# Optimization experiments

Hardware: AMD Instinct MI355X
Metric: run time of the kernel (lower is better)

Reference implementation:

```python
import jax, jax.numpy as jnp
import numpy as np

B, NTS, NOS_F, NTS_F, H, A, HIST = 8192, 64, 7, 6, 64, 9, 2


def _lstm(x, Wih, Whh, bih, bhh):
    # x: [B, T, in] -> all hidden states [B, T, H]; torch gate order (i, f, g, o)
    xg = jnp.einsum('bti,gi->btg', x, Wih) + bih + bhh  # precompute input projection
    Hh = Whh.shape[1]

    def step(carry, xt):
        h, c = carry
        gates = xt + h @ Whh.T
        i, f, g, o = jnp.split(gates, 4, axis=-1)
        c = jax.nn.sigmoid(f) * c + jax.nn.sigmoid(i) * jnp.tanh(g)
        h = jax.nn.sigmoid(o) * jnp.tanh(c)
        return (h, c), h

    z = jnp.zeros((x.shape[0], Hh), x.dtype)
    _, hs = jax.lax.scan(step, (z, z), jnp.swapaxes(xg, 0, 1))
    return jnp.swapaxes(hs, 0, 1)


def _inner(s, WOS, bOS, Wih, Whh, bih, bhh, WTS, bTS):
    # NaN-masked ragged TS sequences + dynamic last-valid-step gather
    b = s.shape[0]
    sOS = s[:, :NOS_F]
    sTS = s[:, NOS_F:].reshape(b, -1, NTS_F)
    nan = jnp.isnan(sTS)
    n = jnp.sum(~nan[:, :, 0], axis=1)          # valid TS count per row
    h_idx = jnp.maximum(n - 1, 0)
    sTS = jnp.where(nan, 0.0, sTS)
    xOS = jax.nn.relu(sOS @ WOS.T + bOS)
    hs = _lstm(sTS, Wih, Whh, bih, bhh)
    xTS = hs[jnp.arange(b), h_idx]              # hidden state at last valid step
    xTS = jax.nn.relu(xTS @ WTS.T + bTS)
    return jnp.concatenate([xOS, xTS], axis=1)  # [B, 128]


def setup_inputs() -> dict:
    key = jax.random.key(0)
    ks = iter(jax.random.split(key, 48))

    def nanify(x, k):  # NaN-pad beyond a random valid prefix length in [1, NTS]
        lens = jax.random.randint(k, x.shape[:-2], 1, NTS + 1)
        mask = jnp.arange(NTS) < lens[..., None]
        return jnp.where(mask[..., None], x, jnp.nan)

    sTS = nanify(jax.random.normal(next(ks), (B, NTS, NTS_F)), next(ks))
    s = jnp.concatenate([jax.random.normal(next(ks), (B, NOS_F)), sTS.reshape(B, -1)], axis=1)
    shTS = nanify(jax.random.normal(next(ks), (B, HIST, NTS, NTS_F)), next(ks))
    s_hist = jnp.concatenate([jax.random.normal(next(ks), (B, HIST, NOS_F)), shTS.reshape(B, HIST, -1)], axis=2)
    hist_len = jax.random.randint(next(ks), (B,), 0, HIST + 1)
    a_hist = jnp.zeros((B, HIST, 1), jnp.float32)

    p = lambda *shape: jax.random.normal(next(ks), shape, jnp.float32) * 0.1
    inp = dict(s=s, s_hist=s_hist, a_hist=a_hist, hist_len=hist_len)
    for t in (0, 1, 2):
        inp[f'WOS{t}'] = p(H, NOS_F); inp[f'bOS{t}'] = p(H)
        inp[f'Wih{t}'] = p(4 * H, NTS_F); inp[f'Whh{t}'] = p(4 * H, H)
        inp[f'bih{t}'] = p(4 * H); inp[f'bhh{t}'] = p(4 * H)
        inp[f'WTS{t}'] = p(H, H); inp[f'bTS{t}'] = p(H)
    inp['Wiho'] = p(4 * H, 2 * H); inp['Whho'] = p(4 * H, H)
    inp['biho'] = p(4 * H); inp['bhho'] = p(4 * H)
    inp['W1'] = p(H, H); inp['b1'] = p(H)
    inp['W2'] = p(A, H); inp['b2'] = p(A)
    return inp


def reference(s, s_hist, a_hist, hist_len,
              WOS0, bOS0, Wih0, Whh0, bih0, bhh0, WTS0, bTS0,
              WOS1, bOS1, Wih1, Whh1, bih1, bhh1, WTS1, bTS1,
              WOS2, bOS2, Wih2, Whh2, bih2, bhh2, WTS2, bTS2,
              Wiho, Whho, biho, bhho, W1, b1, W2, b2):
    b = s.shape[0]
    ok2 = (hist_len >= 2)[:, None]
    # torch mutates s_hist[:,0] for hist_len<2; t1_idx==0 there, so s_t1 is also zeroed
    s_t2 = jnp.where(ok2, s_hist[:, 0, :], 0.0)
    t1_idx = jnp.maximum(hist_len - 1, 0)
    s_t1 = jnp.where(ok2, s_hist[jnp.arange(b), t1_idx, :], 0.0)

    x2 = _inner(s_t2, WOS2, bOS2, Wih2, Whh2, bih2, bhh2, WTS2, bTS2)
    x1 = _inner(s_t1, WOS1, bOS1, Wih1, Whh1, bih1, bhh1, WTS1, bTS1)
    x0 = _inner(s, WOS0, bOS0, Wih0, Whh0, bih0, bhh0, WTS0, bTS0)
    x_tilde = jnp.stack([x2, x1, x0], axis=1)  # [B, 3, 128]

    # per-batch torch.roll(shift=hist_len-2): out[t] = in[(t - shift) mod L]
    L = HIST + 1
    shift = hist_len - 2
    idx = (jnp.arange(L)[None, :] - shift[:, None]) % L
    x_tilde = jnp.take_along_axis(x_tilde, idx[:, :, None], axis=1)

    hs = _lstm(x_tilde, Wiho, Whho, biho, bhho)
    hidden = hs[jnp.arange(b), hist_len]
    x = jax.nn.relu(hidden @ W1.T + b1)
    return x @ W2.T + b2
```

## Files before the change

kernel.cpp:

```cpp
#include <hip/hip_runtime.h>
#include <hip/hip_bf16.h>

#define NB 8192
#define SROW 391

#define TW      22848
#define W_WIH   0
#define W_WHH   1536
#define W_BSUM  17920
#define W_WTS   18176
#define W_BTS   22272
#define W_WOS   22336
#define W_BOS   22784
#define W_OUT   68544
#define WO_WIHO 0
#define WO_WHHO 32768
#define WO_BSUM 49152
#define WO_W1   49408
#define WO_B1   53504
#define WO_W2   53568
#define WO_B2   54144
#define WF_TOTAL 122697

typedef unsigned short u16;
typedef __attribute__((ext_vector_type(8))) short short8;
typedef __attribute__((ext_vector_type(4))) float float4v;

#define MFMA16(a, b, c) __builtin_amdgcn_mfma_f32_16x16x32_bf16((a), (b), (c), 0, 0, 0)

__device__ __forceinline__ float bf2f(u16 u){ return __uint_as_float(((unsigned)u) << 16); }
__device__ __forceinline__ u16 f2bf(float f){
  unsigned x = __float_as_uint(f);
  unsigned r = (x + 0x7FFFu + ((x >> 16) & 1u)) >> 16;
  return (u16)r;
}
__device__ __forceinline__ bool isnanf32(float f){
  unsigned x = __float_as_uint(f);
  return (x & 0x7FFFFFFFu) > 0x7F800000u;
}
__device__ __forceinline__ float ldin(const void* p, size_t i, bool isbf){
  if (isbf) return bf2f(((const u16*)p)[i]);
  return ((const float*)p)[i];
}
__device__ __forceinline__ float sigm(float x){ return __fdividef(1.0f, 1.0f + __expf(-x)); }
__device__ __forceinline__ float tanh_f(float x){ return __fdividef(2.0f, 1.0f + __expf(-2.0f * x)) - 1.0f; }

__device__ __forceinline__ bool detect_bf(const void* whh0){
  const u16* u = (const u16*)whh0;
  const int l = threadIdx.x & 63;
  int e = (u[2 * l] >> 7) & 0xFF;
  unsigned long long m = __ballot(e >= 100 && e <= 141);
  return __popcll(m) >= 32;
}

struct Seg { int src; int src2; int soff; int dst; int n; };
struct SegTab { Seg s[35]; };
struct PtrTab { const void* p[36]; };

__global__ __launch_bounds__(256) void kweights(PtrTab P, SegTab S, float* __restrict__ WF,
                                                const void* __restrict__ whh0, int* __restrict__ flag,
                                                int* __restrict__ ghist){
  const bool isbf = detect_bf(whh0);
  if (blockIdx.x == 0){
    if (threadIdx.x == 0) *flag = isbf ? 1 : 0;
    if (threadIdx.x < 195) ghist[threadIdx.x] = 0;
  }
  Seg sg = S.s[blockIdx.x];
  const void* a = P.p[sg.src];
  const void* b = (sg.src2 >= 0) ? P.p[sg.src2] : nullptr;
  for (int i = threadIdx.x; i < sg.n; i += 256){
    float v = ldin(a, sg.soff + i, isbf);
    if (b) v += ldin(b, sg.soff + i, isbf);
    WF[sg.dst + i] = v;
  }
}

__global__ __launch_bounds__(256) void kprep(const void* __restrict__ s,
                                             const void* __restrict__ sh,
                                             const int* __restrict__ hist_len,
                                             const float* __restrict__ WF,
                                             u16* __restrict__ sTx,
                                             int* __restrict__ nar,
                                             u16* __restrict__ xpartT,
                                             const int* __restrict__ flag,
                                             int* __restrict__ ghist,
                                             int* __restrict__ krank){
  __shared__ u16 stage[4][400];
  const bool isbf = (*flag != 0);
  const int t = blockIdx.y;
  const int w = threadIdx.x >> 6;
  const int l = threadIdx.x & 63;
  const int b = blockIdx.x * 4 + w;
  const int hl = hist_len[b];

  const void* base; size_t soff;
  if (t == 0){ base = s; soff = (size_t)b * SROW; }
  else {
    if (hl < 2) return;
    base = sh; soff = ((size_t)b * 2 + ((t == 1) ? 1 : 0)) * SROW;
  }

  float val[7];
  #pragma unroll
  for (int k = 0; k < 7; ++k){
    const int e = k * 64 + l;
    float v = 0.0f;
    if (e < SROW) v = isbf ? bf2f(((const u16*)base)[soff + e]) : ((const float*)base)[soff + e];
    val[k] = v;
  }
  float sOS[7];
  #pragma unroll
  for (int i = 0; i < 7; ++i) sOS[i] = __shfl(val[0], i);

  int n = 0;
  #pragma unroll
  for (int k = 0; k < 7; ++k){
    const int e = k * 64 + l;
    const bool firstf = (e >= 7) && (e < SROW) && ((e - 7) % 6 == 0);
    unsigned long long m = __ballot(firstf && !isnanf32(val[k]));
    n += __popcll(m);
  }

  #pragma unroll
  for (int k = 0; k < 7; ++k){
    const int e = k * 64 + l;
    if (e >= 7 && e < SROW) stage[w][e] = f2bf(isnanf32(val[k]) ? 0.0f : val[k]);
  }

  {
    const int r = l;
    u16 v0 = stage[w][7 + 6 * r],  v1 = stage[w][8 + 6 * r],  v2 = stage[w][9 + 6 * r];
    u16 v3 = stage[w][10 + 6 * r], v4 = stage[w][11 + 6 * r], v5 = stage[w][12 + 6 * r];
    uint4 wv;
    wv.x = (uint)v0 | ((uint)v1 << 16);
    wv.y = (uint)v2 | ((uint)v3 << 16);
    wv.z = (uint)v4 | ((uint)v5 << 16);
    wv.w = 0u;
    *(uint4*)&sTx[((size_t)(t * NB + b) * 64 + r) * 8] = wv;
  }
  if (l == 0){
    nar[t * NB + b] = n;
    const int key = 64 - min(max(n, 0), 64);
    krank[t * NB + b] = atomicAdd(&ghist[t * 65 + key], 1);
  }

  const float* wos = WF + t * TW + W_WOS;
  const float* bos = WF + t * TW + W_BOS;
  float acc = bos[l];
  #pragma unroll
  for (int i = 0; i < 7; ++i) acc = fmaf(wos[l * 7 + i], sOS[i], acc);
  xpartT[((size_t)(t * NB + b)) * 128 + l] = f2bf(fmaxf(acc, 0.0f));
}

__global__ __launch_bounds__(256) void kscatW(const int* __restrict__ hist_len,
                                              const int* __restrict__ nar,
                                              const int* __restrict__ ghist,
                                              const int* __restrict__ krank,
                                              int* __restrict__ idx,
                                              int* __restrict__ cnt){
  __shared__ int o[65];
  const int t = blockIdx.y;
  if (threadIdx.x == 0){
    int acc = 0;
    for (int k = 0; k < 65; ++k){ o[k] = acc; acc += ghist[t * 65 + k]; }
    if (blockIdx.x == 0) cnt[t] = acc;
  }
  __syncthreads();
  for (int i = threadIdx.x; i < 512; i += 256){
    const int b = blockIdx.x * 512 + i;
    if (t > 0 && hist_len[b] < 2) continue;
    const int key = 64 - min(max(nar[t * NB + b], 0), 64);
    idx[t * NB + o[key] + krank[t * NB + b]] = b;
  }
}

__global__ __launch_bounds__(256) void kmainM(const int* __restrict__ nar,
                                              const float* __restrict__ WF,
                                              const u16* __restrict__ sTx,
                                              u16* __restrict__ xpartT,
                                              const int* __restrict__ idx,
                                              const int* __restrict__ cnt,
                                              u16* __restrict__ zxp){
  __shared__ u16 hHi[2][16 * 72];
  __shared__ u16 hLo[2][16 * 72];
  __shared__ float zh[64];
  __shared__ float zg[256];
  const int t = blockIdx.y;
  const float* Wt = WF + t * TW;

  if (blockIdx.x == 0){
    if (t == 0) return;
    const int u = threadIdx.x & 63;
    const int w = threadIdx.x >> 6;
    const int row = w * 64 + u;
    const float* wr = Wt + W_WHH + row * 64;
    const float bsu = Wt[W_BSUM + row];
    if (w == 0) zh[u] = 0.0f;
    float zc = 0.0f;
    __syncthreads();
    for (int step = 0; step < 64; ++step){
      float a0 = 0.0f, a1 = 0.0f, a2 = 0.0f, a3 = 0.0f;
      #pragma unroll
      for (int k = 0; k < 64; k += 4){
        a0 = fmaf(wr[k],     zh[k],     a0);
        a1 = fmaf(wr[k + 1], zh[k + 1], a1);
        a2 = fmaf(wr[k + 2], zh[k + 2], a2);
        a3 = fmaf(wr[k + 3], zh[k + 3], a3);
      }
      zg[row] = bsu + (a0 + a1) + (a2 + a3);
      __syncthreads();
      if (w == 0){
        float gi = zg[u], gf = zg[64 + u], gg = zg[128 + u], go = zg[192 + u];
        zc = sigm(gf) * zc + sigm(gi) * tanh_f(gg);
        zh[u] = sigm(go) * tanh_f(zc);
      }
      __syncthreads();
    }
    if (w == 0){
      float acc = Wt[W_BTS + u];
      const float* wts = Wt + W_WTS + u * 64;
      for (int k = 0; k < 64; ++k) acc = fmaf(wts[k], zh[k], acc);
      zxp[(t - 1) * 128 + 64 + u] = f2bf(fmaxf(acc, 0.0f));
      zxp[(t - 1) * 128 + u]      = f2bf(fmaxf(Wt[W_BOS + u], 0.0f));
    }
    return;
  }

  const int c = cnt[t];
  const int bx = blockIdx.x - 1;
  if (bx * 16 >= c) return;

  const int lane = threadIdx.x & 63;
  const int q    = __builtin_amdgcn_readfirstlane((int)(threadIdx.x >> 6));
  const int nlo  = lane & 15;
  const int quad = lane >> 4;

  for (int i = threadIdx.x; i < 16 * 72; i += 256){ hHi[0][i] = 0; hLo[0][i] = 0; }

  short8 aW[4][2], aX[4];
  float4v binit[4];
  #pragma unroll
  for (int g = 0; g < 4; ++g){
    const int mrow = g * 64 + q * 16 + nlo;
    const float* wr = Wt + W_WHH + mrow * 64;
    #pragma unroll
    for (int f = 0; f < 2; ++f){
      const int k0 = f * 32 + quad * 8;
      short8 a;
      #pragma unroll
      for (int j = 0; j < 8; ++j) a[j] = (short)f2bf(wr[k0 + j]);
      aW[g][f] = a;
    }
    const float* wi = Wt + W_WIH + mrow * 6;
    short8 ax = {0, 0, 0, 0, 0, 0, 0, 0};
    if (quad == 0){
      #pragma unroll
      for (int j = 0; j < 6; ++j) ax[j] = (short)f2bf(wi[j]);
    }
    aX[g] = ax;
    binit[g] = *(const float4v*)(Wt + W_BSUM + g * 64 + q * 16 + quad * 4);
  }

  const int pos = min(bx * 16 + nlo, c - 1);
  const int bb = idx[t * NB + pos];
  const int n_l = nar[t * NB + bb];
  const u16* sB = sTx + (size_t)(t * NB + bb) * 512;
  int nmax = n_l;
  #pragma unroll
  for (int o = 1; o < 16; o <<= 1) nmax = max(nmax, __shfl_xor(nmax, o));

  float c_st[4], h_st[4];
  #pragma unroll
  for (int r = 0; r < 4; ++r){ c_st[r] = 0.0f; h_st[r] = 0.0f; }

  short8 xcur = {0, 0, 0, 0, 0, 0, 0, 0}, xnxt;
  if (lane < 16) xcur = *(const short8*)sB;

  __syncthreads();

  for (int step = 0; step < nmax; ++step){
    xnxt = (short8){0, 0, 0, 0, 0, 0, 0, 0};
    const int ns = min(step + 1, 63);
    if (lane < 16) xnxt = *(const short8*)(sB + (size_t)ns * 8);

    const u16* rHi = hHi[step & 1];
    const u16* rLo = hLo[step & 1];
    u16* wHi = hHi[(step + 1) & 1];
    u16* wLo = hLo[(step + 1) & 1];

    const int hb = nlo * 72 + quad * 8;
    short8 h0 = *(const short8*)&rHi[hb];
    short8 h1 = *(const short8*)&rHi[hb + 32];
    short8 l0 = *(const short8*)&rLo[hb];
    short8 l1 = *(const short8*)&rLo[hb + 32];

    float4v acc[4];
    #pragma unroll
    for (int g = 0; g < 4; ++g){
      float4v a = binit[g];
      a = MFMA16(aX[g], xcur, a);
      a = MFMA16(aW[g][0], h0, a);
      a = MFMA16(aW[g][1], h1, a);
      a = MFMA16(aW[g][0], l0, a);
      a = MFMA16(aW[g][1], l1, a);
      acc[g] = a;
    }

    const bool v = (step < n_l);
    u16 hb4[4], lb4[4];
    #pragma unroll
    for (int r = 0; r < 4; ++r){
      float gi = acc[0][r], gf = acc[1][r], gg = acc[2][r], go = acc[3][r];
      float cn = sigm(gf) * c_st[r] + sigm(gi) * tanh_f(gg);
      float hn = sigm(go) * tanh_f(cn);
      c_st[r] = v ? cn : c_st[r];
      h_st[r] = v ? hn : h_st[r];
      u16 hi = f2bf(h_st[r]);
      float lo = h_st[r] - bf2f(hi);
      hb4[r] = hi; lb4[r] = f2bf(lo);
    }
    const int off = nlo * 72 + q * 16 + quad * 4;
    uint2 hw, lw;
    hw.x = (uint)hb4[0] | ((uint)hb4[1] << 16);
    hw.y = (uint)hb4[2] | ((uint)hb4[3] << 16);
    lw.x = (uint)lb4[0] | ((uint)lb4[1] << 16);
    lw.y = (uint)lb4[2] | ((uint)lb4[3] << 16);
    *(uint2*)&wHi[off] = hw;
    *(uint2*)&wLo[off] = lw;

    xcur = xnxt;
    __syncthreads();
  }

  const u16* fHi = hHi[nmax & 1];
  const u16* fLo = hLo[nmax & 1];
  short8 aT[2];
  #pragma unroll
  for (int f = 0; f < 2; ++f){
    const float* wr = Wt + W_WTS + (q * 16 + nlo) * 64 + f * 32 + quad * 8;
    short8 a;
    #pragma unroll
    for (int j = 0; j < 8; ++j) a[j] = (short)f2bf(wr[j]);
    aT[f] = a;
  }
  float4v btsv = *(const float4v*)(Wt + W_BTS + q * 16 + quad * 4);
  {
    const int hb = nlo * 72 + quad * 8;
    float4v a = btsv;
    a = MFMA16(aT[0], *(const short8*)&fHi[hb], a);
    a = MFMA16(aT[1], *(const short8*)&fHi[hb + 32], a);
    a = MFMA16(aT[0], *(const short8*)&fLo[hb], a);
    a = MFMA16(aT[1], *(const short8*)&fLo[hb + 32], a);
    u16 o4[4];
    #pragma unroll
    for (int r = 0; r < 4; ++r) o4[r] = f2bf(fmaxf(a[r], 0.0f));
    size_t oidx = ((size_t)(t * NB + bb)) * 128 + 64 + q * 16 + quad * 4;
    uint2 wv;
    wv.x = (uint)o4[0] | ((uint)o4[1] << 16);
    wv.y = (uint)o4[2] | ((uint)o4[3] << 16);
    *(uint2*)&xpartT[oidx] = wv;
  }
}

__global__ __launch_bounds__(256) void kfinalM(const float* __restrict__ WF,
                                               const u16* __restrict__ xpartT,
                                               const u16* __restrict__ zxp,
                                               const int* __restrict__ hist_len,
                                               void* __restrict__ out,
                                               const int* __restrict__ flag){
  __shared__ u16 hHi[32 * 72];
  __shared__ u16 hLo[32 * 72];
  __shared__ float x1T[32 * 68];
  const bool isbf = (*flag != 0);
  const int b0   = blockIdx.x * 32;
  const int lane = threadIdx.x & 63;
  const int q    = __builtin_amdgcn_readfirstlane((int)(threadIdx.x >> 6));
  const int nlo  = lane & 15;
  const int quad = lane >> 4;

  for (int i = threadIdx.x; i < 32 * 72; i += 256){ hHi[i] = 0; hLo[i] = 0; }

  const float* WO = WF + W_OUT;
  int hl2[2];
  #pragma unroll
  for (int nt = 0; nt < 2; ++nt) hl2[nt] = hist_len[b0 + nt * 16 + nlo];

  short8 aI[4][4], aH[4][2];
  float4v bi4[4];
  #pragma unroll
  for (int g = 0; g < 4; ++g){
    const int mrow = g * 64 + q * 16 + nlo;
    #pragma unroll
    for (int f = 0; f < 4; ++f){
      const float* w = WO + WO_WIHO + mrow * 128 + f * 32 + quad * 8;
      short8 a;
      #pragma unroll
      for (int j = 0; j < 8; ++j) a[j] = (short)f2bf(w[j]);
      aI[g][f] = a;
    }
    #pragma unroll
    for (int f = 0; f < 2; ++f){
      const float* w = WO + WO_WHHO + mrow * 64 + f * 32 + quad * 8;
      short8 a;
      #pragma unroll
      for (int j = 0; j < 8; ++j) a[j] = (short)f2bf(w[j]);
      aH[g][f] = a;
    }
    bi4[g] = *(const float4v*)(WO + WO_BSUM + g * 64 + q * 16 + quad * 4);
  }

  float c_st[2][4], h_st[2][4];
  #pragma unroll
  for (int nt = 0; nt < 2; ++nt)
    #pragma unroll
    for (int r = 0; r < 4; ++r){ c_st[nt][r] = 0.0f; h_st[nt][r] = 0.0f; }
  __syncthreads();

  for (int p = 0; p < 3; ++p){
    float4v acc[4][2];
    #pragma unroll
    for (int nt = 0; nt < 2; ++nt){
      const int bb = b0 + nt * 16 + nlo;
      const int tt = 2 - ((p - hl2[nt] + 2) % 3);
      const u16* xb = (tt > 0 && hl2[nt] < 2) ? (zxp + (tt - 1) * 128)
                                              : xpartT + ((size_t)(tt * NB + bb)) * 128;
      short8 xf[4];
      #pragma unroll
      for (int f = 0; f < 4; ++f) xf[f] = *(const short8*)(xb + f * 32 + quad * 8);
      const int hb = (nt * 16 + nlo) * 72 + quad * 8;
      short8 h0 = *(const short8*)&hHi[hb];
      short8 h1 = *(const short8*)&hHi[hb + 32];
      short8 l0 = *(const short8*)&hLo[hb];
      short8 l1 = *(const short8*)&hLo[hb + 32];
      #pragma unroll
      for (int g = 0; g < 4; ++g){
        float4v a = bi4[g];
        #pragma unroll
        for (int f = 0; f < 4; ++f) a = MFMA16(aI[g][f], xf[f], a);
        a = MFMA16(aH[g][0], h0, a);
        a = MFMA16(aH[g][1], h1, a);
        a = MFMA16(aH[g][0], l0, a);
        a = MFMA16(aH[g][1], l1, a);
        acc[g][nt] = a;
      }
    }
    __syncthreads();
    #pragma unroll
    for (int nt = 0; nt < 2; ++nt){
      const bool v = (p <= hl2[nt]);
      u16 hb4[4], lb4[4];
      #pragma unroll
      for (int r = 0; r < 4; ++r){
        float gi = acc[0][nt][r], gf = acc[1][nt][r], gg = acc[2][nt][r], go = acc[3][nt][r];
        float cn = sigm(gf) * c_st[nt][r] + sigm(gi) * tanh_f(gg);
        float hn = sigm(go) * tanh_f(cn);
        c_st[nt][r] = v ? cn : c_st[nt][r];
        h_st[nt][r] = v ? hn : h_st[nt][r];
        u16 hi = f2bf(h_st[nt][r]);
        float lo = h_st[nt][r] - bf2f(hi);
        hb4[r] = hi; lb4[r] = f2bf(lo);
      }
      const int off = (nt * 16 + nlo) * 72 + q * 16 + quad * 4;
      uint2 hw, lw;
      hw.x = (uint)hb4[0] | ((uint)hb4[1] << 16);
      hw.y = (uint)hb4[2] | ((uint)hb4[3] << 16);
      lw.x = (uint)lb4[0] | ((uint)lb4[1] << 16);
      lw.y = (uint)lb4[2] | ((uint)lb4[3] << 16);
      *(uint2*)&hHi[off] = hw;
      *(uint2*)&hLo[off] = lw;
    }
    __syncthreads();
  }

  short8 a1[2];
  #pragma unroll
  for (int f = 0; f < 2; ++f){
    const float* w = WO + WO_W1 + (q * 16 + nlo) * 64 + f * 32 + quad * 8;
    short8 a;
    #pragma unroll
    for (int j = 0; j < 8; ++j) a[j] = (short)f2bf(w[j]);
    a1[f] = a;
  }
  float4v b1v = *(const float4v*)(WO + WO_B1 + q * 16 + quad * 4);
  #pragma unroll
  for (int nt = 0; nt < 2; ++nt){
    const int hb = (nt * 16 + nlo) * 72 + quad * 8;
    float4v a = b1v;
    a = MFMA16(a1[0], *(const short8*)&hHi[hb], a);
    a = MFMA16(a1[1], *(const short8*)&hHi[hb + 32], a);
    a = MFMA16(a1[0], *(const short8*)&hLo[hb], a);
    a = MFMA16(a1[1], *(const short8*)&hLo[hb + 32], a);
    float4v rv;
    #pragma unroll
    for (int r = 0; r < 4; ++r) rv[r] = fmaxf(a[r], 0.0f);
    *(float4v*)&x1T[(nt * 16 + nlo) * 68 + q * 16 + quad * 4] = rv;
  }
  __syncthreads();

  const int bloc = threadIdx.x >> 3;
  const int r0 = threadIdx.x & 7;
  const float* w2 = WO + WO_W2;
  const float* b2 = WO + WO_B2;
  for (int r = r0; r < 9; r += 8){
    float acc = b2[r];
    const float* wr = w2 + r * 64;
    #pragma unroll
    for (int k = 0; k < 64; ++k) acc = fmaf(wr[k], x1T[bloc * 68 + k], acc);
    if (isbf) ((u16*)out)[(size_t)(b0 + bloc) * 9 + r] = f2bf(acc);
    else      ((float*)out)[(size_t)(b0 + bloc) * 9 + r] = acc;
  }
}

extern "C" void kernel_launch(void* const* d_in, const int* in_sizes, int n_in,
                              void* d_out, int out_size, void* d_ws, size_t ws_size,
                              hipStream_t stream){
  char* ws = (char*)d_ws;
  float* WF = (float*)ws;
  size_t off = ((size_t)WF_TOTAL * 4 + 255) & ~(size_t)255;
  u16* sTx = (u16*)(ws + off);    off += (size_t)3 * NB * 512 * 2;
  u16* xpartT = (u16*)(ws + off); off += (size_t)3 * NB * 128 * 2;
  int* nar = (int*)(ws + off);    off += (size_t)3 * NB * 4;
  int* flag = (int*)(ws + off);   off += 256;
  int* cnt  = (int*)(ws + off);   off += 256;
  int* ghist = (int*)(ws + off);  off += 3 * 65 * 4 + 64;
  int* idx  = (int*)(ws + off);   off += (size_t)3 * NB * 4;
  int* krank = (int*)(ws + off);  off += (size_t)3 * NB * 4;
  u16* zxp  = (u16*)(ws + off);   off += 2 * 128 * 2;

  PtrTab P;
  for (int i = 0; i < 36; ++i) P.p[i] = d_in[i];

  SegTab S;
  int si = 0;
  for (int t = 0; t < 3; ++t){
    int base = 4 + 8 * t;
    int d = t * TW;
    S.s[si++] = { base + 2, -1,       0,     d + W_WIH,         1536 };
    S.s[si++] = { base + 3, -1,       0,     d + W_WHH,         8192 };
    S.s[si++] = { base + 3, -1,       8192,  d + W_WHH + 8192,  8192 };
    S.s[si++] = { base + 4, base + 5, 0,     d + W_BSUM,        256  };
    S.s[si++] = { base + 6, -1,       0,     d + W_WTS,         4096 };
    S.s[si++] = { base + 7, -1,       0,     d + W_BTS,         64   };
    S.s[si++] = { base + 0, -1,       0,     d + W_WOS,         448  };
    S.s[si++] = { base + 1, -1,       0,     d + W_BOS,         64   };
  }
  {
    int O = W_OUT;
    for (int k = 0; k < 4; ++k)
      S.s[si++] = { 28, -1, k * 8192, O + WO_WIHO + k * 8192, 8192 };
    S.s[si++] = { 29, -1, 0,    O + WO_WHHO,        8192 };
    S.s[si++] = { 29, -1, 8192, O + WO_WHHO + 8192, 8192 };
    S.s[si++] = { 30, 31, 0,    O + WO_BSUM,        256  };
    S.s[si++] = { 32, -1, 0,    O + WO_W1,          4096 };
    S.s[si++] = { 33, -1, 0,    O + WO_B1,          64   };
    S.s[si++] = { 34, -1, 0,    O + WO_W2,          576  };
    S.s[si++] = { 35, -1, 0,    O + WO_B2,          9    };
  }

  const int* hl_ptr = (const int*)d_in[3];

  kweights<<<dim3(35), 256, 0, stream>>>(P, S, WF, d_in[7], flag, ghist);
  kprep<<<dim3(NB / 4, 3), 256, 0, stream>>>(d_in[0], d_in[1], hl_ptr, WF, sTx, nar, xpartT, flag, ghist, krank);
  kscatW<<<dim3(16, 3), 256, 0, stream>>>(hl_ptr, nar, ghist, krank, idx, cnt);
  kmainM<<<dim3(513, 3), 256, 0, stream>>>(nar, WF, sTx, xpartT, idx, cnt, zxp);
  kfinalM<<<dim3(NB / 32), 256, 0, stream>>>(WF, xpartT, zxp, hl_ptr, d_out, flag);
}
```

Measured before the change: 367.7 us.

## Run each 16-sequence LSTM tile in a single wavefront, removing block barriers

The main LSTM kernel moves from four wavefronts per 16-sequence tile to one. That wavefront holds all 16 gate-row weight fragments in registers and swaps MFMA operand roles so the hidden state is the A operand. The bias is folded into the input MFMA through constant-one input columns. Hidden-state exchange goes through LDS inside the single wave, so the per-step __syncthreads disappears. The zero-input path is also restructured to one wave. The risks are heavy register pressure from 48 short8 weight fragments with launch_bounds(64,1), and four times as many MFMAs serialized per wave, which may lower occupancy and latency hiding.

```diff
diff --git a/kernel.cpp b/kernel.cpp
--- a/kernel.cpp
+++ b/kernel.cpp
@@ -174,191 +174,201 @@
   }
 }
 
-__global__ __launch_bounds__(256) void kmainM(const int* __restrict__ nar,
-                                              const float* __restrict__ WF,
-                                              const u16* __restrict__ sTx,
-                                              u16* __restrict__ xpartT,
-                                              const int* __restrict__ idx,
-                                              const int* __restrict__ cnt,
-                                              u16* __restrict__ zxp){
-  __shared__ u16 hHi[2][16 * 72];
-  __shared__ u16 hLo[2][16 * 72];
-  __shared__ float zh[64];
-  __shared__ float zg[256];
+__global__ __launch_bounds__(64, 1) void kmainW(const int* __restrict__ nar,
+                                                const float* __restrict__ WF,
+                                                const u16* __restrict__ sTx,
+                                                u16* __restrict__ xpartT,
+                                                const int* __restrict__ idx,
+                                                const int* __restrict__ cnt,
+                                                u16* __restrict__ zxp){
+  __shared__ u16 hsc[2][16 * 104];
+  __shared__ float zsh[64];
   const int t = blockIdx.y;
   const float* Wt = WF + t * TW;
+  const int lane = threadIdx.x & 63;
+  const int quad = lane >> 4;
+  const int col  = lane & 15;
 
   if (blockIdx.x == 0){
     if (t == 0) return;
-    const int u = threadIdx.x & 63;
-    const int w = threadIdx.x >> 6;
-    const int row = w * 64 + u;
-    const float* wr = Wt + W_WHH + row * 64;
-    const float bsu = Wt[W_BSUM + row];
-    if (w == 0) zh[u] = 0.0f;
-    float zc = 0.0f;
-    __syncthreads();
+    const int u = lane;
+    const float* w0 = Wt + W_WHH + u * 64;
+    const float* w1 = Wt + W_WHH + (64 + u) * 64;
+    const float* w2 = Wt + W_WHH + (128 + u) * 64;
+    const float* w3 = Wt + W_WHH + (192 + u) * 64;
+    const float b0 = Wt[W_BSUM + u], b1 = Wt[W_BSUM + 64 + u];
+    const float b2 = Wt[W_BSUM + 128 + u], b3 = Wt[W_BSUM + 192 + u];
+    float zc = 0.0f, zh = 0.0f;
     for (int step = 0; step < 64; ++step){
-      float a0 = 0.0f, a1 = 0.0f, a2 = 0.0f, a3 = 0.0f;
-      #pragma unroll
-      for (int k = 0; k < 64; k += 4){
-        a0 = fmaf(wr[k],     zh[k],     a0);
-        a1 = fmaf(wr[k + 1], zh[k + 1], a1);
-        a2 = fmaf(wr[k + 2], zh[k + 2], a2);
-        a3 = fmaf(wr[k + 3], zh[k + 3], a3);
-      }
-      zg[row] = bsu + (a0 + a1) + (a2 + a3);
-      __syncthreads();
-      if (w == 0){
-        float gi = zg[u], gf = zg[64 + u], gg = zg[128 + u], go = zg[192 + u];
-        zc = sigm(gf) * zc + sigm(gi) * tanh_f(gg);
-        zh[u] = sigm(go) * tanh_f(zc);
-      }
-      __syncthreads();
-    }
-    if (w == 0){
-      float acc = Wt[W_BTS + u];
-      const float* wts = Wt + W_WTS + u * 64;
-      for (int k = 0; k < 64; ++k) acc = fmaf(wts[k], zh[k], acc);
-      zxp[(t - 1) * 128 + 64 + u] = f2bf(fmaxf(acc, 0.0f));
-      zxp[(t - 1) * 128 + u]      = f2bf(fmaxf(Wt[W_BOS + u], 0.0f));
-    }
+      zsh[u] = zh;
+      float g0 = b0, g1 = b1, g2 = b2, g3 = b3;
+      for (int k = 0; k < 64; ++k){
+        const float hv = zsh[k];
+        g0 = fmaf(w0[k], hv, g0);
+        g1 = fmaf(w1[k], hv, g1);
+        g2 = fmaf(w2[k], hv, g2);
+        g3 = fmaf(w3[k], hv, g3);
+      }
+      zc = sigm(g1) * zc + sigm(g0) * tanh_f(g2);
+      zh = sigm(g3) * tanh_f(zc);
+    }
+    zsh[u] = zh;
+    float acc = Wt[W_BTS + u];
+    const float* wts = Wt + W_WTS + u * 64;
+    for (int k = 0; k < 64; ++k) acc = fmaf(wts[k], zsh[k], acc);
+    zxp[(t - 1) * 128 + 64 + u] = f2bf(fmaxf(acc, 0.0f));
+    zxp[(t - 1) * 128 + u]      = f2bf(fmaxf(Wt[W_BOS + u], 0.0f));
     return;
   }
 
   const int c = cnt[t];
-  const int bx = blockIdx.x - 1;
-  if (bx * 16 >= c) return;
-
-  const int lane = threadIdx.x & 63;
-  const int q    = __builtin_amdgcn_readfirstlane((int)(threadIdx.x >> 6));
-  const int nlo  = lane & 15;
-  const int quad = lane >> 4;
-
-  for (int i = threadIdx.x; i < 16 * 72; i += 256){ hHi[0][i] = 0; hLo[0][i] = 0; }
-
-  short8 aW[4][2], aX[4];
-  float4v binit[4];
+  const int tid = blockIdx.x - 1;
+  if (tid * 16 >= c) return;
+
+  const int posA = min(tid * 16 + col, c - 1);
+  const int bbA  = idx[t * NB + posA];
+  const int nA   = nar[t * NB + bbA];
+  int nv[4], bbD[4];
+  #pragma unroll
+  for (int r = 0; r < 4; ++r){
+    nv[r]  = __shfl(nA, quad * 4 + r);
+    bbD[r] = __shfl(bbA, quad * 4 + r);
+  }
+  int nmax = nA;
+  #pragma unroll
+  for (int o = 1; o < 16; o <<= 1) nmax = max(nmax, __shfl_xor(nmax, o));
+
+  short8 BW[16][2];
+  short8 BX[16];
+  #pragma unroll
+  for (int g = 0; g < 16; ++g){
+    #pragma unroll
+    for (int kf = 0; kf < 2; ++kf){
+      short8 a;
+      #pragma unroll
+      for (int j = 0; j < 8; ++j){
+        const int hd = (j & 3) * 16 + kf * 8 + quad * 2 + (j >> 2);
+        a[j] = (short)f2bf(Wt[W_WHH + (g * 16 + col) * 64 + hd]);
+      }
+      BW[g][kf] = a;
+    }
+    short8 x = {0, 0, 0, 0, 0, 0, 0, 0};
+    if (quad == 0){
+      #pragma unroll
+      for (int j = 0; j < 6; ++j) x[j] = (short)f2bf(Wt[W_WIH + (g * 16 + col) * 6 + j]);
+      const float bs = Wt[W_BSUM + g * 16 + col];
+      const u16 bh = f2bf(bs);
+      x[6] = (short)bh;
+      x[7] = (short)f2bf(bs - bf2f(bh));
+    }
+    BX[g] = x;
+  }
+
+  for (int i = lane; i < 16 * 104; i += 64){ hsc[0][i] = 0; hsc[1][i] = 0; }
+
+  const u16* sBA = sTx + (size_t)(t * NB + bbA) * 512;
+  short8 xcur = *(const short8*)sBA;
+  xcur[6] = (short)0x3F80; xcur[7] = (short)0x3F80;
+
+  const short8 z8 = {0, 0, 0, 0, 0, 0, 0, 0};
+  short8 AHh0 = z8, AHh1 = z8, AHl0 = z8, AHl1 = z8;
+  float cst[4][4];
+  #pragma unroll
+  for (int hf = 0; hf < 4; ++hf)
+    #pragma unroll
+    for (int r = 0; r < 4; ++r) cst[hf][r] = 0.0f;
+  const float4v zf = {0.0f, 0.0f, 0.0f, 0.0f};
+
+  char* hiW = (char*)&hsc[0][0];
+  char* loW = (char*)&hsc[1][0];
+
+  for (int step = 0; step < nmax; ++step){
+    short8 xn = *(const short8*)(sBA + (size_t)min(step + 1, 63) * 8);
+
+    #pragma unroll
+    for (int p = 0; p < 2; ++p){
+      float4v ac[2][4];
+      #pragma unroll
+      for (int hh = 0; hh < 2; ++hh){
+        const int hf = p * 2 + hh;
+        #pragma unroll
+        for (int gg = 0; gg < 4; ++gg){
+          const int g = gg * 4 + hf;
+          float4v a = MFMA16(xcur, BX[g], zf);
+          a = MFMA16(AHh0, BW[g][0], a);
+          a = MFMA16(AHh1, BW[g][1], a);
+          a = MFMA16(AHl0, BW[g][0], a);
+          a = MFMA16(AHl1, BW[g][1], a);
+          ac[hh][gg] = a;
+        }
+      }
+      #pragma unroll
+      for (int r = 0; r < 4; ++r){
+        float hn2[2];
+        #pragma unroll
+        for (int hh = 0; hh < 2; ++hh){
+          const int hf = p * 2 + hh;
+          const float gi = ac[hh][0][r], gf = ac[hh][1][r];
+          const float gG = ac[hh][2][r], go = ac[hh][3][r];
+          const float cn = sigm(gf) * cst[hf][r] + sigm(gi) * tanh_f(gG);
+          const float hn = sigm(go) * tanh_f(cn);
+          const bool v = (step < nv[r]);
+          cst[hf][r] = v ? cn : cst[hf][r];
+          hn2[hh] = hn;
+        }
+        if (step < nv[r]){
+          const u16 h0 = f2bf(hn2[0]), h1 = f2bf(hn2[1]);
+          const u16 l0 = f2bf(hn2[0] - bf2f(h0)), l1 = f2bf(hn2[1] - bf2f(h1));
+          const int byteoff = (quad * 4 + r) * 208 + col * 8 + p * 4;
+          *(uint*)(hiW + byteoff) = (uint)h0 | ((uint)h1 << 16);
+          *(uint*)(loW + byteoff) = (uint)l0 | ((uint)l1 << 16);
+        }
+      }
+    }
+    {
+      const char* hb = hiW + col * 208;
+      const char* lb = loW + col * 208;
+      AHh0 = *(const short8*)(hb + quad * 16);
+      AHh1 = *(const short8*)(hb + 64 + quad * 16);
+      AHl0 = *(const short8*)(lb + quad * 16);
+      AHl1 = *(const short8*)(lb + 64 + quad * 16);
+    }
+    xcur = xn;
+    xcur[6] = (short)0x3F80; xcur[7] = (short)0x3F80;
+  }
+
+  short8 xone = z8;
+  xone[6] = (short)0x3F80; xone[7] = (short)0x3F80;
   #pragma unroll
   for (int g = 0; g < 4; ++g){
-    const int mrow = g * 64 + q * 16 + nlo;
-    const float* wr = Wt + W_WHH + mrow * 64;
-    #pragma unroll
-    for (int f = 0; f < 2; ++f){
-      const int k0 = f * 32 + quad * 8;
+    short8 bt0, bt1;
+    #pragma unroll
+    for (int kf = 0; kf < 2; ++kf){
       short8 a;
       #pragma unroll
-      for (int j = 0; j < 8; ++j) a[j] = (short)f2bf(wr[k0 + j]);
-      aW[g][f] = a;
-    }
-    const float* wi = Wt + W_WIH + mrow * 6;
-    short8 ax = {0, 0, 0, 0, 0, 0, 0, 0};
+      for (int j = 0; j < 8; ++j){
+        const int hd = (j & 3) * 16 + kf * 8 + quad * 2 + (j >> 2);
+        a[j] = (short)f2bf(Wt[W_WTS + (g * 16 + col) * 64 + hd]);
+      }
+      if (kf == 0) bt0 = a; else bt1 = a;
+    }
+    short8 btx = z8;
     if (quad == 0){
-      #pragma unroll
-      for (int j = 0; j < 6; ++j) ax[j] = (short)f2bf(wi[j]);
-    }
-    aX[g] = ax;
-    binit[g] = *(const float4v*)(Wt + W_BSUM + g * 64 + q * 16 + quad * 4);
-  }
-
-  const int pos = min(bx * 16 + nlo, c - 1);
-  const int bb = idx[t * NB + pos];
-  const int n_l = nar[t * NB + bb];
-  const u16* sB = sTx + (size_t)(t * NB + bb) * 512;
-  int nmax = n_l;
-  #pragma unroll
-  for (int o = 1; o < 16; o <<= 1) nmax = max(nmax, __shfl_xor(nmax, o));
-
-  float c_st[4], h_st[4];
-  #pragma unroll
-  for (int r = 0; r < 4; ++r){ c_st[r] = 0.0f; h_st[r] = 0.0f; }
-
-  short8 xcur = {0, 0, 0, 0, 0, 0, 0, 0}, xnxt;
-  if (lane < 16) xcur = *(const short8*)sB;
-
-  __syncthreads();
-
-  for (int step = 0; step < nmax; ++step){
-    xnxt = (short8){0, 0, 0, 0, 0, 0, 0, 0};
-    const int ns = min(step + 1, 63);
-    if (lane < 16) xnxt = *(const short8*)(sB + (size_t)ns * 8);
-
-    const u16* rHi = hHi[step & 1];
-    const u16* rLo = hLo[step & 1];
-    u16* wHi = hHi[(step + 1) & 1];
-    u16* wLo = hLo[(step + 1) & 1];
-
-    const int hb = nlo * 72 + quad * 8;
-    short8 h0 = *(const short8*)&rHi[hb];
-    short8 h1 = *(const short8*)&rHi[hb + 32];
-    short8 l0 = *(const short8*)&rLo[hb];
-    short8 l1 = *(const short8*)&rLo[hb + 32];
-
-    float4v acc[4];
-    #pragma unroll
-    for (int g = 0; g < 4; ++g){
-      float4v a = binit[g];
-      a = MFMA16(aX[g], xcur, a);
-      a = MFMA16(aW[g][0], h0, a);
-      a = MFMA16(aW[g][1], h1, a);
-      a = MFMA16(aW[g][0], l0, a);
-      a = MFMA16(aW[g][1], l1, a);
-      acc[g] = a;
-    }
-
-    const bool v = (step < n_l);
-    u16 hb4[4], lb4[4];
+      const float bs = Wt[W_BTS + g * 16 + col];
+      const u16 bh = f2bf(bs);
+      btx[6] = (short)bh;
+      btx[7] = (short)f2bf(bs - bf2f(bh));
+    }
+    float4v a = MFMA16(xone, btx, zf);
+    a = MFMA16(AHh0, bt0, a);
+    a = MFMA16(AHh1, bt1, a);
+    a = MFMA16(AHl0, bt0, a);
+    a = MFMA16(AHl1, bt1, a);
     #pragma unroll
     for (int r = 0; r < 4; ++r){
-      float gi = acc[0][r], gf = acc[1][r], gg = acc[2][r], go = acc[3][r];
-      float cn = sigm(gf) * c_st[r] + sigm(gi) * tanh_f(gg);
-      float hn = sigm(go) * tanh_f(cn);
-      c_st[r] = v ? cn : c_st[r];
-      h_st[r] = v ? hn : h_st[r];
-      u16 hi = f2bf(h_st[r]);
-      float lo = h_st[r] - bf2f(hi);
-      hb4[r] = hi; lb4[r] = f2bf(lo);
-    }
-    const int off = nlo * 72 + q * 16 + quad * 4;
-    uint2 hw, lw;
-    hw.x = (uint)hb4[0] | ((uint)hb4[1] << 16);
-    hw.y = (uint)hb4[2] | ((uint)hb4[3] << 16);
-    lw.x = (uint)lb4[0] | ((uint)lb4[1] << 16);
-    lw.y = (uint)lb4[2] | ((uint)lb4[3] << 16);
-    *(uint2*)&wHi[off] = hw;
-    *(uint2*)&wLo[off] = lw;
-
-    xcur = xnxt;
-    __syncthreads();
-  }
-
-  const u16* fHi = hHi[nmax & 1];
-  const u16* fLo = hLo[nmax & 1];
-  short8 aT[2];
-  #pragma unroll
-  for (int f = 0; f < 2; ++f){
-    const float* wr = Wt + W_WTS + (q * 16 + nlo) * 64 + f * 32 + quad * 8;
-    short8 a;
-    #pragma unroll
-    for (int j = 0; j < 8; ++j) a[j] = (short)f2bf(wr[j]);
-    aT[f] = a;
-  }
-  float4v btsv = *(const float4v*)(Wt + W_BTS + q * 16 + quad * 4);
-  {
-    const int hb = nlo * 72 + quad * 8;
-    float4v a = btsv;
-    a = MFMA16(aT[0], *(const short8*)&fHi[hb], a);
-    a = MFMA16(aT[1], *(const short8*)&fHi[hb + 32], a);
-    a = MFMA16(aT[0], *(const short8*)&fLo[hb], a);
-    a = MFMA16(aT[1], *(const short8*)&fLo[hb + 32], a);
-    u16 o4[4];
-    #pragma unroll
-    for (int r = 0; r < 4; ++r) o4[r] = f2bf(fmaxf(a[r], 0.0f));
-    size_t oidx = ((size_t)(t * NB + bb)) * 128 + 64 + q * 16 + quad * 4;
-    uint2 wv;
-    wv.x = (uint)o4[0] | ((uint)o4[1] << 16);
-    wv.y = (uint)o4[2] | ((uint)o4[3] << 16);
-    *(uint2*)&xpartT[oidx] = wv;
+      const float ov = fmaxf(a[r], 0.0f);
+      xpartT[((size_t)(t * NB + bbD[r])) * 128 + 64 + g * 16 + col] = f2bf(ov);
+    }
   }
 }
 
@@ -562,6 +572,6 @@
   kweights<<<dim3(35), 256, 0, stream>>>(P, S, WF, d_in[7], flag, ghist);
   kprep<<<dim3(NB / 4, 3), 256, 0, stream>>>(d_in[0], d_in[1], hl_ptr, WF, sTx, nar, xpartT, flag, ghist, krank);
   kscatW<<<dim3(16, 3), 256, 0, stream>>>(hl_ptr, nar, ghist, krank, idx, cnt);
-  kmainM<<<dim3(513, 3), 256, 0, stream>>>(nar, WF, sTx, xpartT, idx, cnt, zxp);
+  kmainW<<<dim3(513, 3), 64, 0, stream>>>(nar, WF, sTx, xpartT, idx, cnt, zxp);
   kfinalM<<<dim3(NB / 32), 256, 0, stream>>>(WF, xpartT, zxp, hl_ptr, d_out, flag);
 }
```

After: 475.3 us. +29.3%, slower.

## Prepack bf16 MFMA weight fragments once and use packed bf16 conversion

Applied to the files above, without the earlier changes.

Adds a kfrag kernel that converts the fp32 weights once into bf16 laid out in per-lane MFMA fragment order. kmainM and kfinalM then load each fragment with a single 16-byte read instead of each block doing strided fp32 loads plus software rounding. The per-step hi/lo split of the hidden state now uses the v_cvt_pk_bf16_f32 instruction in place of manual rounding. The cost is an extra kernel launch and workspace buffer, and the hardware conversion's rounding could differ slightly from the software round-to-nearest-even.

```diff
diff --git a/kernel.cpp b/kernel.cpp
--- a/kernel.cpp
+++ b/kernel.cpp
@@ -22,6 +22,14 @@
 #define WO_B2   54144
 #define WF_TOTAL 122697
 
+#define OFF_WHH   0
+#define OFF_WIH   49152
+#define OFF_WTS   73728
+#define OFF_WIHO  86016
+#define OFF_WHHO  118784
+#define OFF_W1    135168
+#define FB_TOTAL  139264
+
 typedef unsigned short u16;
 typedef __attribute__((ext_vector_type(8))) short short8;
 typedef __attribute__((ext_vector_type(4))) float float4v;
@@ -33,6 +41,11 @@
   unsigned x = __float_as_uint(f);
   unsigned r = (x + 0x7FFFu + ((x >> 16) & 1u)) >> 16;
   return (u16)r;
+}
+__device__ __forceinline__ unsigned cvtpk_bf16(float a, float b){
+  unsigned r;
+  asm("v_cvt_pk_bf16_f32 %0, %1, %2" : "=v"(r) : "v"(a), "v"(b));
+  return r;
 }
 __device__ __forceinline__ bool isnanf32(float f){
   unsigned x = __float_as_uint(f);
@@ -73,6 +86,63 @@
     if (b) v += ldin(b, sg.soff + i, isbf);
     WF[sg.dst + i] = v;
   }
+}
+
+__global__ __launch_bounds__(256) void kfrag(const float* __restrict__ WF, u16* __restrict__ FB){
+  const int i = blockIdx.x * 256 + threadIdx.x;
+  short8 v = {0, 0, 0, 0, 0, 0, 0, 0};
+  int dst;
+  if (i < 6144){
+    const int lane = i & 63, f = (i >> 6) & 1, g = (i >> 7) & 3, q = (i >> 9) & 3, t = i >> 11;
+    const int mrow = g * 64 + q * 16 + (lane & 15);
+    const float* src = WF + t * TW + W_WHH + mrow * 64 + f * 32 + (lane >> 4) * 8;
+    #pragma unroll
+    for (int j = 0; j < 8; ++j) v[j] = (short)f2bf(src[j]);
+    dst = OFF_WHH + i * 8;
+  } else if (i < 9216){
+    const int k = i - 6144;
+    const int lane = k & 63, g = (k >> 6) & 3, q = (k >> 8) & 3, t = k >> 10;
+    if ((lane >> 4) == 0){
+      const int mrow = g * 64 + q * 16 + (lane & 15);
+      const float* src = WF + t * TW + W_WIH + mrow * 6;
+      #pragma unroll
+      for (int j = 0; j < 6; ++j) v[j] = (short)f2bf(src[j]);
+    }
+    dst = OFF_WIH + k * 8;
+  } else if (i < 10752){
+    const int k = i - 9216;
+    const int lane = k & 63, f = (k >> 6) & 1, q = (k >> 7) & 3, t = k >> 9;
+    const int row = q * 16 + (lane & 15);
+    const float* src = WF + t * TW + W_WTS + row * 64 + f * 32 + (lane >> 4) * 8;
+    #pragma unroll
+    for (int j = 0; j < 8; ++j) v[j] = (short)f2bf(src[j]);
+    dst = OFF_WTS + k * 8;
+  } else if (i < 14848){
+    const int k = i - 10752;
+    const int lane = k & 63, f = (k >> 6) & 3, g = (k >> 8) & 3, q = (k >> 10) & 3;
+    const int mrow = g * 64 + q * 16 + (lane & 15);
+    const float* src = WF + W_OUT + WO_WIHO + mrow * 128 + f * 32 + (lane >> 4) * 8;
+    #pragma unroll
+    for (int j = 0; j < 8; ++j) v[j] = (short)f2bf(src[j]);
+    dst = OFF_WIHO + k * 8;
+  } else if (i < 16896){
+    const int k = i - 14848;
+    const int lane = k & 63, f = (k >> 6) & 1, g = (k >> 7) & 3, q = (k >> 9) & 3;
+    const int mrow = g * 64 + q * 16 + (lane & 15);
+    const float* src = WF + W_OUT + WO_WHHO + mrow * 64 + f * 32 + (lane >> 4) * 8;
+    #pragma unroll
+    for (int j = 0; j < 8; ++j) v[j] = (short)f2bf(src[j]);
+    dst = OFF_WHHO + k * 8;
+  } else {
+    const int k = i - 16896;
+    const int lane = k & 63, f = (k >> 6) & 1, q = (k >> 7) & 3;
+    const int row = q * 16 + (lane & 15);
+    const float* src = WF + W_OUT + WO_W1 + row * 64 + f * 32 + (lane >> 4) * 8;
+    #pragma unroll
+    for (int j = 0; j < 8; ++j) v[j] = (short)f2bf(src[j]);
+    dst = OFF_W1 + k * 8;
+  }
+  *(short8*)&FB[dst] = v;
 }
 
 __global__ __launch_bounds__(256) void kprep(const void* __restrict__ s,
@@ -176,6 +246,7 @@
 
 __global__ __launch_bounds__(256) void kmainM(const int* __restrict__ nar,
                                               const float* __restrict__ WF,
+                                              const u16* __restrict__ FB,
                                               const u16* __restrict__ sTx,
                                               u16* __restrict__ xpartT,
                                               const int* __restrict__ idx,
@@ -241,23 +312,10 @@
   float4v binit[4];
   #pragma unroll
   for (int g = 0; g < 4; ++g){
-    const int mrow = g * 64 + q * 16 + nlo;
-    const float* wr = Wt + W_WHH + mrow * 64;
-    #pragma unroll
-    for (int f = 0; f < 2; ++f){
-      const int k0 = f * 32 + quad * 8;
-      short8 a;
-      #pragma unroll
-      for (int j = 0; j < 8; ++j) a[j] = (short)f2bf(wr[k0 + j]);
-      aW[g][f] = a;
-    }
-    const float* wi = Wt + W_WIH + mrow * 6;
-    short8 ax = {0, 0, 0, 0, 0, 0, 0, 0};
-    if (quad == 0){
-      #pragma unroll
-      for (int j = 0; j < 6; ++j) ax[j] = (short)f2bf(wi[j]);
-    }
-    aX[g] = ax;
+    #pragma unroll
+    for (int f = 0; f < 2; ++f)
+      aW[g][f] = *(const short8*)&FB[OFF_WHH + (((((t * 4 + q) * 4 + g) * 2 + f) * 64 + lane)) * 8];
+    aX[g] = *(const short8*)&FB[OFF_WIH + ((((t * 4 + q) * 4 + g) * 64 + lane)) * 8];
     binit[g] = *(const float4v*)(Wt + W_BSUM + g * 64 + q * 16 + quad * 4);
   }
 
@@ -307,7 +365,6 @@
     }
 
     const bool v = (step < n_l);
-    u16 hb4[4], lb4[4];
     #pragma unroll
     for (int r = 0; r < 4; ++r){
       float gi = acc[0][r], gf = acc[1][r], gg = acc[2][r], go = acc[3][r];
@@ -315,16 +372,19 @@
       float hn = sigm(go) * tanh_f(cn);
       c_st[r] = v ? cn : c_st[r];
       h_st[r] = v ? hn : h_st[r];
-      u16 hi = f2bf(h_st[r]);
-      float lo = h_st[r] - bf2f(hi);
-      hb4[r] = hi; lb4[r] = f2bf(lo);
     }
+    const unsigned hx = cvtpk_bf16(h_st[0], h_st[1]);
+    const unsigned hy = cvtpk_bf16(h_st[2], h_st[3]);
+    const float g0 = __uint_as_float(hx << 16);
+    const float g1 = __uint_as_float(hx & 0xFFFF0000u);
+    const float g2 = __uint_as_float(hy << 16);
+    const float g3 = __uint_as_float(hy & 0xFFFF0000u);
+    const unsigned lx = cvtpk_bf16(h_st[0] - g0, h_st[1] - g1);
+    const unsigned ly = cvtpk_bf16(h_st[2] - g2, h_st[3] - g3);
     const int off = nlo * 72 + q * 16 + quad * 4;
     uint2 hw, lw;
-    hw.x = (uint)hb4[0] | ((uint)hb4[1] << 16);
-    hw.y = (uint)hb4[2] | ((uint)hb4[3] << 16);
-    lw.x = (uint)lb4[0] | ((uint)lb4[1] << 16);
-    lw.y = (uint)lb4[2] | ((uint)lb4[3] << 16);
+    hw.x = hx; hw.y = hy;
+    lw.x = lx; lw.y = ly;
     *(uint2*)&wHi[off] = hw;
     *(uint2*)&wLo[off] = lw;
 
@@ -336,13 +396,8 @@
   const u16* fLo = hLo[nmax & 1];
   short8 aT[2];
   #pragma unroll
-  for (int f = 0; f < 2; ++f){
-    const float* wr = Wt + W_WTS + (q * 16 + nlo) * 64 + f * 32 + quad * 8;
-    short8 a;
-    #pragma unroll
-    for (int j = 0; j < 8; ++j) a[j] = (short)f2bf(wr[j]);
-    aT[f] = a;
-  }
+  for (int f = 0; f < 2; ++f)
+    aT[f] = *(const short8*)&FB[OFF_WTS + ((((t * 4 + q) * 2 + f) * 64 + lane)) * 8];
   float4v btsv = *(const float4v*)(Wt + W_BTS + q * 16 + quad * 4);
   {
     const int hb = nlo * 72 + quad * 8;
@@ -363,6 +418,7 @@
 }
 
 __global__ __launch_bounds__(256) void kfinalM(const float* __restrict__ WF,
+                                               const u16* __restrict__ FB,
                                                const u16* __restrict__ xpartT,
                                                const u16* __restrict__ zxp,
                                                const int* __restrict__ hist_len,
@@ -389,23 +445,12 @@
   float4v bi4[4];
   #pragma unroll
   for (int g = 0; g < 4; ++g){
-    const int mrow = g * 64 + q * 16 + nlo;
-    #pragma unroll
-    for (int f = 0; f < 4; ++f){
-      const float* w = WO + WO_WIHO + mrow * 128 + f * 32 + quad * 8;
-      short8 a;
-      #pragma unroll
-      for (int j = 0; j < 8; ++j) a[j] = (short)f2bf(w[j]);
-      aI[g][f] = a;
-    }
-    #pragma unroll
-    for (int f = 0; f < 2; ++f){
-      const float* w = WO + WO_WHHO + mrow * 64 + f * 32 + quad * 8;
-      short8 a;
-      #pragma unroll
-      for (int j = 0; j < 8; ++j) a[j] = (short)f2bf(w[j]);
-      aH[g][f] = a;
-    }
+    #pragma unroll
+    for (int f = 0; f < 4; ++f)
+      aI[g][f] = *(const short8*)&FB[OFF_WIHO + ((((q * 4 + g) * 4 + f) * 64 + lane)) * 8];
+    #pragma unroll
+    for (int f = 0; f < 2; ++f)
+      aH[g][f] = *(const short8*)&FB[OFF_WHHO + ((((q * 4 + g) * 2 + f) * 64 + lane)) * 8];
     bi4[g] = *(const float4v*)(WO + WO_BSUM + g * 64 + q * 16 + quad * 4);
   }
 
@@ -448,7 +493,6 @@
     #pragma unroll
     for (int nt = 0; nt < 2; ++nt){
       const bool v = (p <= hl2[nt]);
-      u16 hb4[4], lb4[4];
       #pragma unroll
       for (int r = 0; r < 4; ++r){
         float gi = acc[0][nt][r], gf = acc[1][nt][r], gg = acc[2][nt][r], go = acc[3][nt][r];
@@ -456,16 +500,19 @@
         float hn = sigm(go) * tanh_f(cn);
         c_st[nt][r] = v ? cn : c_st[nt][r];
         h_st[nt][r] = v ? hn : h_st[nt][r];
-        u16 hi = f2bf(h_st[nt][r]);
-        float lo = h_st[nt][r] - bf2f(hi);
-        hb4[r] = hi; lb4[r] = f2bf(lo);
       }
+      const unsigned hx = cvtpk_bf16(h_st[nt][0], h_st[nt][1]);
+      const unsigned hy = cvtpk_bf16(h_st[nt][2], h_st[nt][3]);
+      const float g0 = __uint_as_float(hx << 16);
+      const float g1 = __uint_as_float(hx & 0xFFFF0000u);
+      const float g2 = __uint_as_float(hy << 16);
+      const float g3 = __uint_as_float(hy & 0xFFFF0000u);
+      const unsigned lx = cvtpk_bf16(h_st[nt][0] - g0, h_st[nt][1] - g1);
+      const unsigned ly = cvtpk_bf16(h_st[nt][2] - g2, h_st[nt][3] - g3);
       const int off = (nt * 16 + nlo) * 72 + q * 16 + quad * 4;
       uint2 hw, lw;
-      hw.x = (uint)hb4[0] | ((uint)hb4[1] << 16);
-      hw.y = (uint)hb4[2] | ((uint)hb4[3] << 16);
-      lw.x = (uint)lb4[0] | ((uint)lb4[1] << 16);
-      lw.y = (uint)lb4[2] | ((uint)lb4[3] << 16);
+      hw.x = hx; hw.y = hy;
+      lw.x = lx; lw.y = ly;
       *(uint2*)&hHi[off] = hw;
       *(uint2*)&hLo[off] = lw;
     }
@@ -474,13 +521,8 @@
 
   short8 a1[2];
   #pragma unroll
-  for (int f = 0; f < 2; ++f){
-    const float* w = WO + WO_W1 + (q * 16 + nlo) * 64 + f * 32 + quad * 8;
-    short8 a;
-    #pragma unroll
-    for (int j = 0; j < 8; ++j) a[j] = (short)f2bf(w[j]);
-    a1[f] = a;
-  }
+  for (int f = 0; f < 2; ++f)
+    a1[f] = *(const short8*)&FB[OFF_W1 + (((q * 2 + f) * 64 + lane)) * 8];
   float4v b1v = *(const float4v*)(WO + WO_B1 + q * 16 + quad * 4);
   #pragma unroll
   for (int nt = 0; nt < 2; ++nt){
@@ -526,6 +568,7 @@
   int* idx  = (int*)(ws + off);   off += (size_t)3 * NB * 4;
   int* krank = (int*)(ws + off);  off += (size_t)3 * NB * 4;
   u16* zxp  = (u16*)(ws + off);   off += 2 * 128 * 2;
+  u16* FB   = (u16*)(ws + off);   off += (size_t)FB_TOTAL * 2;
 
   PtrTab P;
   for (int i = 0; i < 36; ++i) P.p[i] = d_in[i];
@@ -560,8 +603,9 @@
   const int* hl_ptr = (const int*)d_in[3];
 
   kweights<<<dim3(35), 256, 0, stream>>>(P, S, WF, d_in[7], flag, ghist);
+  kfrag<<<dim3(68), 256, 0, stream>>>(WF, FB);
   kprep<<<dim3(NB / 4, 3), 256, 0, stream>>>(d_in[0], d_in[1], hl_ptr, WF, sTx, nar, xpartT, flag, ghist, krank);
   kscatW<<<dim3(16, 3), 256, 0, stream>>>(hl_ptr, nar, ghist, krank, idx, cnt);
-  kmainM<<<dim3(513, 3), 256, 0, stream>>>(nar, WF, sTx, xpartT, idx, cnt, zxp);
-  kfinalM<<<dim3(NB / 32), 256, 0, stream>>>(WF, xpartT, zxp, hl_ptr, d_out, flag);
-}
+  kmainM<<<dim3(513, 3), 256, 0, stream>>>(nar, WF, FB, sTx, xpartT, idx, cnt, zxp);
+  kfinalM<<<dim3(NB / 32), 256, 0, stream>>>(WF, FB, xpartT, zxp, hl_ptr, d_out, flag);
+}
```

Result: faster. 357.5 us (-2.8%).
